# Optimization experiments

Measured on AMD Instinct MI355X. Metric: run time of the kernel, lower is better.

The kernel has to match this reference:

```python
import jax, jax.numpy as jnp
import numpy as np

BETA = 4.0  # temperature of soft cluster assignment in filling loss


def _pairwise_sq_dist(a, b):
    # a: [N,D], b: [K,D] -> [N,K] squared euclidean distances
    return (jnp.sum(a * a, -1, keepdims=True)
            - 2.0 * (a @ b.T)
            + jnp.sum(b * b, -1)[None, :])


def setup_inputs() -> dict:
    key = jax.random.key(0)
    k1, k2, k3, k4 = jax.random.split(key, 4)
    N, D, K = 131072, 64, 16
    x = jax.random.normal(k1, (N, D), jnp.float32)
    cluster_centers = jax.random.normal(k2, (K, D), jnp.float32)
    target = jax.random.normal(k3, (N, D), jnp.float32)
    ft = jax.random.uniform(k4, (K,), jnp.float32)
    filling_target = ft / ft.sum()
    # prediction = kmeans assignment of the fixed target set (computed once, constant)
    prediction = jnp.argmin(_pairwise_sq_dist(target, cluster_centers), axis=-1)
    return {"x": x, "cluster_centers": cluster_centers,
            "filling_target": filling_target, "target": target,
            "prediction": prediction}


def reference(x, cluster_centers, filling_target, target, prediction):
    N, D = x.shape
    Nt = target.shape[0]
    K = cluster_centers.shape[0]
    BIG = jnp.finfo(x.dtype).max  # padding value that sorts to the end

    d2 = _pairwise_sq_dist(x, cluster_centers)  # [N,K]

    # --- cluster filling MSE: soft assignment fractions vs filling_target ---
    soft = jax.nn.softmax(-BETA * d2, axis=-1)          # [N,K]
    filling = soft.mean(axis=0)                          # [K]
    loss_fil = jnp.mean((filling - filling_target) ** 2)

    # --- per-cluster sorted (per-dimension 1D) Wasserstein distance ---
    pred_x = jax.lax.stop_gradient(jnp.argmin(d2, axis=-1))  # kmeans_predict(x).detach()
    L = min(N, Nt)  # static upper bound on per-cluster min_size
    rows = jnp.arange(L)

    loss_med = jnp.zeros((), x.dtype)
    for k in range(K):  # fixed structural loop over clusters
        mx = pred_x == k
        mt = prediction == k
        m = jnp.minimum(mx.sum(), mt.sum())  # min_size (dynamic value, static shapes)
        # keep only the FIRST m members (original order), as x[in_cluster][:m]
        keep_x = mx & ((jnp.cumsum(mx) - 1) < m)
        keep_t = mt & ((jnp.cumsum(mt) - 1) < m)
        # mask out non-members with BIG so they sort to the bottom, sort per dim
        xs = jnp.sort(jnp.where(keep_x[:, None], x, BIG), axis=0)[:L]       # [L,D]
        ts = jnp.sort(jnp.where(keep_t[:, None], target, BIG), axis=0)[:L]  # [L,D]
        valid = (rows < m)[:, None]                                          # [L,1]
        diff = jnp.where(valid, jnp.abs(xs - ts), 0.0)
        # mean(|sort(x) - sort(y)|) over the m x D selected elements
        denom = (m * D).astype(x.dtype)
        loss_med = loss_med + jnp.where(m > 0, diff.sum() / denom, 0.0)

    return loss_fil + loss_med
```

## Files before the change

### kernel.cpp

```cpp
#include <hip/hip_runtime.h>
#include <stdint.h>

#define N_ROWS 131072
#define DIMS 64
#define KCL 16
#define BETA 4.0f
#define NBLK 512
#define CHUNK 16384
#define STH 1024
#define SEG_STRIDE 263168
#define VOFF (1u<<21)

typedef unsigned long long u64;
typedef unsigned int u32;

__device__ __forceinline__ u32 enc_f(float f) {
  u32 u = __float_as_uint(f);
  return (u & 0x80000000u) ? ~u : (u | 0x80000000u);
}
__device__ __forceinline__ float dec_f(u32 e) {
  u32 u = (e & 0x80000000u) ? (e & 0x7FFFFFFFu) : ~e;
  return __uint_as_float(u);
}
__device__ __forceinline__ u32 U4(u32 u) { return u ^ ((u >> 3) & 7u); }

#define CS(a,b,dd) { u32 _mn = min(a,b), _mx = max(a,b); a = (dd)?_mn:_mx; b = (dd)?_mx:_mn; }
#define CSV(A,B,D) { CS(A.x,B.x,D) CS(A.y,B.y,D) CS(A.z,B.z,D) CS(A.w,B.w,D) }

#define M16G(a,b,c,d,e,f,g,h,i2,j2,k2,l,m,n,o,p,D) \
  CS(a,i2,D) CS(b,j2,D) CS(c,k2,D) CS(d,l,D) CS(e,m,D) CS(f,n,D) CS(g,o,D) CS(h,p,D) \
  CS(a,e,D)  CS(b,f,D)  CS(c,g,D)  CS(d,h,D) CS(i2,m,D) CS(j2,n,D) CS(k2,o,D) CS(l,p,D) \
  CS(a,c,D)  CS(b,d,D)  CS(e,g,D)  CS(f,h,D) CS(i2,k2,D) CS(j2,l,D) CS(m,o,D) CS(n,p,D) \
  CS(a,b,D)  CS(c,d,D)  CS(e,f,D)  CS(g,h,D) CS(i2,j2,D) CS(k2,l,D) CS(m,n,D) CS(o,p,D)

#define SORT16G(a,b,c,d,e,f,g,h,i2,j2,k2,l,m,n,o,p,D) \
  CS(a,b,D) CS(c,d,!(D)) CS(e,f,D) CS(g,h,!(D)) CS(i2,j2,D) CS(k2,l,!(D)) CS(m,n,D) CS(o,p,!(D)) \
  CS(a,c,D) CS(b,d,D) CS(e,g,!(D)) CS(f,h,!(D)) CS(i2,k2,D) CS(j2,l,D) CS(m,o,!(D)) CS(n,p,!(D)) \
  CS(a,b,D) CS(c,d,D) CS(e,f,!(D)) CS(g,h,!(D)) CS(i2,j2,D) CS(k2,l,D) CS(m,n,!(D)) CS(o,p,!(D)) \
  CS(a,e,D) CS(b,f,D) CS(c,g,D) CS(d,h,D) CS(i2,m,!(D)) CS(j2,n,!(D)) CS(k2,o,!(D)) CS(l,p,!(D)) \
  CS(a,c,D) CS(b,d,D) CS(e,g,D) CS(f,h,D) CS(i2,k2,!(D)) CS(j2,l,!(D)) CS(m,o,!(D)) CS(n,p,!(D)) \
  CS(a,b,D) CS(c,d,D) CS(e,f,D) CS(g,h,D) CS(i2,j2,!(D)) CS(k2,l,!(D)) CS(m,n,!(D)) CS(o,p,!(D)) \
  M16G(a,b,c,d,e,f,g,h,i2,j2,k2,l,m,n,o,p,D)

#define MERGE16F(D) M16G(r0,r1,r2,r3,r4,r5,r6,r7,r8,r9,r10,r11,r12,r13,r14,r15,D)
#define SORT16F(D)  SORT16G(r0,r1,r2,r3,r4,r5,r6,r7,r8,r9,r10,r11,r12,r13,r14,r15,D)

#define LOADTILE16(src) \
  { uint4 _a0=src[U4(ub+0)],_a1=src[U4(ub+1)],_a2=src[U4(ub+2)],_a3=src[U4(ub+3)]; \
    r0=_a0.x;r1=_a0.y;r2=_a0.z;r3=_a0.w; r4=_a1.x;r5=_a1.y;r6=_a1.z;r7=_a1.w; \
    r8=_a2.x;r9=_a2.y;r10=_a2.z;r11=_a2.w; r12=_a3.x;r13=_a3.y;r14=_a3.z;r15=_a3.w; }

#define STORETILE16(dst) \
  { dst[U4(ub+0)]=make_uint4(r0,r1,r2,r3);   dst[U4(ub+1)]=make_uint4(r4,r5,r6,r7); \
    dst[U4(ub+2)]=make_uint4(r8,r9,r10,r11); dst[U4(ub+3)]=make_uint4(r12,r13,r14,r15); }

__device__ __forceinline__ void wave_tail(uint4* lds4, u32 RU, u32 Lw, u32 gbase,
                                          u32 k, u32 jtop, u32 lane)
{
  u32 j = jtop;
  while (j >= 32u) {
    u32 ud = j >> 3;
    if (lane < (Lw >> 4)) {
      u32 bu = RU + (((lane & ~(ud - 1u)) << 2) | (lane & (ud - 1u)));
      bool up = (((gbase + (bu << 2)) & k) == 0u);
      uint4 A0 = lds4[U4(bu)],           A1 = lds4[U4(bu + ud)],
            A2 = lds4[U4(bu + 2u * ud)], A3 = lds4[U4(bu + 3u * ud)];
      CSV(A0,A2,up) CSV(A1,A3,up)
      CSV(A0,A1,up) CSV(A2,A3,up)
      lds4[U4(bu)] = A0;           lds4[U4(bu + ud)] = A1;
      lds4[U4(bu + 2u * ud)] = A2; lds4[U4(bu + 3u * ud)] = A3;
    }
    j >>= 2;
  }
  if (j == 16u) {
    u32 total = Lw >> 3;
    for (u32 inst = lane; inst < total; inst += 64u) {
      u32 bu = RU + (((inst & ~3u) << 1) | (inst & 3u));
      bool up = (((gbase + (bu << 2)) & k) == 0u);
      uint4 A = lds4[U4(bu)], B = lds4[U4(bu + 4u)];
      CSV(A,B,up)
      lds4[U4(bu)] = A; lds4[U4(bu + 4u)] = B;
    }
  }
}

__device__ __forceinline__ void cross1(uint4* lds4, u32 Wn, u32 gb, u32 k, u32 jtop, u32 tid)
{
  u32 ud = jtop >> 2;
  u32 total = Wn >> 3;
  for (u32 inst = tid; inst < total; inst += STH) {
    u32 bu = ((inst & ~(ud - 1u)) << 1) | (inst & (ud - 1u));
    bool up = (((gb + (bu << 2)) & k) == 0u);
    uint4 A = lds4[U4(bu)], B = lds4[U4(bu + ud)];
    CSV(A,B,up)
    lds4[U4(bu)] = A; lds4[U4(bu + ud)] = B;
  }
}
__device__ __forceinline__ void cross2(uint4* lds4, u32 Wn, u32 gb, u32 k, u32 jtop, u32 tid)
{
  u32 ud = jtop >> 3;
  u32 total = Wn >> 4;
  for (u32 inst = tid; inst < total; inst += STH) {
    u32 bu = ((inst & ~(ud - 1u)) << 2) | (inst & (ud - 1u));
    bool up = (((gb + (bu << 2)) & k) == 0u);
    uint4 A0 = lds4[U4(bu)],            A1 = lds4[U4(bu + ud)],
          A2 = lds4[U4(bu + 2u * ud)],  A3 = lds4[U4(bu + 3u * ud)];
    CSV(A0,A2,up) CSV(A1,A3,up)
    CSV(A0,A1,up) CSV(A2,A3,up)
    lds4[U4(bu)] = A0;           lds4[U4(bu + ud)] = A1;
    lds4[U4(bu + 2u * ud)] = A2; lds4[U4(bu + 3u * ud)] = A3;
  }
}
__device__ __forceinline__ void cross3(uint4* lds4, u32 Wn, u32 gb, u32 k, u32 jtop, u32 tid)
{
  u32 ud = jtop >> 4;
  u32 total = Wn >> 5;
  for (u32 inst = tid; inst < total; inst += STH) {
    u32 bu = ((inst & ~(ud - 1u)) << 3) | (inst & (ud - 1u));
    bool up = (((gb + (bu << 2)) & k) == 0u);
    uint4 A0 = lds4[U4(bu)],            A1 = lds4[U4(bu + ud)],
          A2 = lds4[U4(bu + 2u * ud)],  A3 = lds4[U4(bu + 3u * ud)],
          A4 = lds4[U4(bu + 4u * ud)],  A5 = lds4[U4(bu + 5u * ud)],
          A6 = lds4[U4(bu + 6u * ud)],  A7 = lds4[U4(bu + 7u * ud)];
    CSV(A0,A4,up) CSV(A1,A5,up) CSV(A2,A6,up) CSV(A3,A7,up)
    CSV(A0,A2,up) CSV(A1,A3,up) CSV(A4,A6,up) CSV(A5,A7,up)
    CSV(A0,A1,up) CSV(A2,A3,up) CSV(A4,A5,up) CSV(A6,A7,up)
    lds4[U4(bu)] = A0;           lds4[U4(bu + ud)] = A1;
    lds4[U4(bu + 2u * ud)] = A2; lds4[U4(bu + 3u * ud)] = A3;
    lds4[U4(bu + 4u * ud)] = A4; lds4[U4(bu + 5u * ud)] = A5;
    lds4[U4(bu + 6u * ud)] = A6; lds4[U4(bu + 7u * ud)] = A7;
  }
}

__global__ __launch_bounds__(256) void k_assign(
    const float* __restrict__ x, const float* __restrict__ centers,
    const int* __restrict__ predT, int* __restrict__ predX,
    float* __restrict__ fill_sum, u32* __restrict__ histX, u32* __restrict__ histT)
{
  __shared__ float c[KCL][DIMS];
  __shared__ float cn[KCL];
  __shared__ float fs[KCL];
  __shared__ u32 hx[KCL], ht[KCL];
  int tid = threadIdx.x;
  for (int t = tid; t < KCL * DIMS; t += 256) c[t / DIMS][t % DIMS] = centers[t];
  if (tid < KCL) { fs[tid] = 0.f; hx[tid] = 0; ht[tid] = 0; }
  __syncthreads();
  if (tid < KCL) {
    float s = 0.f;
    for (int d = 0; d < DIMS; ++d) s += c[tid][d] * c[tid][d];
    cn[tid] = s;
  }
  __syncthreads();
  int i = blockIdx.x * 256 + tid;
  const float4* xr = (const float4*)(x + (size_t)i * DIMS);
  float dot[KCL];
#pragma unroll
  for (int k = 0; k < KCL; ++k) dot[k] = 0.f;
  for (int t = 0; t < DIMS / 4; ++t) {
    float4 v = xr[t];
#pragma unroll
    for (int k = 0; k < KCL; ++k)
      dot[k] += v.x * c[k][4 * t] + v.y * c[k][4 * t + 1] + v.z * c[k][4 * t + 2] + v.w * c[k][4 * t + 3];
  }
  float sc[KCL];
  float smin = 3.0e38f; int kmin = 0;
#pragma unroll
  for (int k = 0; k < KCL; ++k) {
    sc[k] = cn[k] - 2.f * dot[k];
    if (sc[k] < smin) { smin = sc[k]; kmin = k; }
  }
  float e[KCL]; float esum = 0.f;
#pragma unroll
  for (int k = 0; k < KCL; ++k) { e[k] = expf(-BETA * (sc[k] - smin)); esum += e[k]; }
  float inv = 1.f / esum;
#pragma unroll
  for (int k = 0; k < KCL; ++k) atomicAdd(&fs[k], e[k] * inv);
  predX[i] = kmin;
  atomicAdd(&hx[kmin], 1u);
  atomicAdd(&ht[predT[i]], 1u);
  __syncthreads();
  if (tid < KCL) {
    histX[blockIdx.x * KCL + tid] = hx[tid];
    histT[blockIdx.x * KCL + tid] = ht[tid];
    atomicAdd(&fill_sum[tid], fs[tid]);
  }
}

__global__ __launch_bounds__(512) void k_scan(
    const u32* __restrict__ histX, const u32* __restrict__ histT,
    u32* __restrict__ baseX, u32* __restrict__ baseT,
    const float* __restrict__ fill_sum, const float* __restrict__ ftarget,
    int* __restrict__ m_out, float* __restrict__ w_out,
    int* __restrict__ p_out, int* __restrict__ pOff_out, int* __restrict__ mOff_out,
    int* __restrict__ nlo_out, float* __restrict__ loss_fil)
{
  __shared__ u32 part[2][KCL][17];
  __shared__ u32 tot[2][KCL];
  __shared__ float sq[KCL];
  __shared__ int sp[KCL];
  __shared__ int smv[KCL];
  int tid = threadIdx.x;
  int side = tid >> 8;
  int rem = tid & 255;
  int c = rem >> 4;
  int sub = rem & 15;
  const u32* hist = side ? histT : histX;
  u32* base = side ? baseT : baseX;
  int b0 = sub * 32;
  u32 s = 0;
  for (int b = b0; b < b0 + 32; ++b) s += hist[b * KCL + c];
  part[side][c][sub] = s;
  __syncthreads();
  if (sub == 0) {
    u32 run = 0;
    for (int t = 0; t < 16; ++t) { u32 v = part[side][c][t]; part[side][c][t] = run; run += v; }
    tot[side][c] = run;
  }
  __syncthreads();
  u32 run = part[side][c][sub];
  for (int b = b0; b < b0 + 32; ++b) { base[b * KCL + c] = run; run += hist[b * KCL + c]; }
  if (tid < KCL) {
    int m = min((int)tot[0][tid], (int)tot[1][tid]);
    m_out[tid] = m;
    smv[tid] = m;
    w_out[tid] = (m > 0) ? 1.f / ((float)m * (float)DIMS) : 0.f;
    int pp = 32;
    while (pp < m) pp <<= 1;
    sp[tid] = pp;
    p_out[tid] = pp;
    int nlo = 0;
    if (pp > CHUNK) {
      int nch = pp / CHUNK;
      for (int j = 1; j < nch; j += 2) {
        int v = m - j * CHUNK;
        if (v < 0) v = 0;
        if (v > CHUNK) v = CHUNK;
        nlo += CHUNK - v;
      }
    }
    nlo_out[tid] = nlo;
    float d = fill_sum[tid] / (float)N_ROWS - ftarget[tid];
    sq[tid] = d * d;
  }
  __syncthreads();
  if (tid == 0) {
    float s2 = 0.f;
    int acc = 0, macc = 0;
    for (int k = 0; k < KCL; ++k) {
      s2 += sq[k];
      pOff_out[k] = acc;
      acc += sp[k];
      mOff_out[k] = macc;
      macc += smv[k];
    }
    pOff_out[KCL] = acc;
    mOff_out[KCL] = macc;
    *loss_fil = s2 / (float)KCL;
  }
}

__global__ __launch_bounds__(256) void k_rank(
    const int* __restrict__ predX, const int* __restrict__ predT,
    const u32* __restrict__ baseX, const u32* __restrict__ baseT,
    const int* __restrict__ mG, const int* __restrict__ mOffG,
    int* __restrict__ idxX, int* __restrict__ idxT)
{
  __shared__ int wcX[4][KCL], wcT[4][KCL];
  __shared__ int smo[KCL], sm2[KCL];
  int tid = threadIdx.x;
  int lane = tid & 63, wave = tid >> 6;
  if (tid < KCL) { smo[tid] = mOffG[tid]; sm2[tid] = mG[tid]; }
  int i = blockIdx.x * 256 + tid;
  int kx = predX[i], kt = predT[i];
  u64 below = (1ull << lane) - 1ull;
  int lrX = 0, lrT = 0;
  for (int cc = 0; cc < KCL; ++cc) {
    u64 mx = __ballot(kx == cc);
    u64 mt = __ballot(kt == cc);
    if (kx == cc) lrX = __popcll(mx & below);
    if (kt == cc) lrT = __popcll(mt & below);
    if (lane == 0) { wcX[wave][cc] = __popcll(mx); wcT[wave][cc] = __popcll(mt); }
  }
  __syncthreads();
  int wbX = 0, wbT = 0;
  for (int w2 = 0; w2 < wave; ++w2) { wbX += wcX[w2][kx]; wbT += wcT[w2][kt]; }
  int rX = (int)baseX[blockIdx.x * KCL + kx] + wbX + lrX;
  int rT = (int)baseT[blockIdx.x * KCL + kt] + wbT + lrT;
  if (rX < sm2[kx]) idxX[smo[kx] + rX] = i;
  if (rT < sm2[kt]) idxT[smo[kt] + rT] = i;
}

__global__ __launch_bounds__(256) void k_gather(
    const float* __restrict__ x, const float* __restrict__ tgt,
    const int* __restrict__ idxX, const int* __restrict__ idxT,
    const int* __restrict__ pOffG, const int* __restrict__ mOffG,
    const int* __restrict__ mG, const int* __restrict__ pG,
    u32* __restrict__ valX, u32* __restrict__ valT, int d0, int Dbc)
{
  __shared__ int spOff[KCL + 1];
  __shared__ int smo[KCL], sm2[KCL], sp2[KCL];
  int tid = threadIdx.x;
  if (tid <= KCL) spOff[tid] = pOffG[tid];
  if (tid < KCL) { smo[tid] = mOffG[tid]; sm2[tid] = mG[tid]; sp2[tid] = pG[tid]; }
  __syncthreads();
  int pos = blockIdx.x * 256 + tid;
  if (pos >= spOff[KCL]) return;
  int c = 0;
#pragma unroll
  for (int cc = 1; cc < KCL; ++cc) c += (pos >= spOff[cc]) ? 1 : 0;
  int rel = pos - spOff[c];
  u32* dx = valX + pos;
  u32* dt = valT + pos;
  if (rel < sm2[c]) {
    int w = smo[c] + rel;
    int iX = idxX[w], iT = idxT[w];
    if ((Dbc & 3) == 0) {
      const float4* xr = (const float4*)(x + (size_t)iX * DIMS + d0);
      const float4* tr = (const float4*)(tgt + (size_t)iT * DIMS + d0);
      for (int q = 0; q < (Dbc >> 2); ++q) {
        float4 a = xr[q];
        float4 b = tr[q];
        size_t base = (size_t)(4 * q) * SEG_STRIDE;
        dx[base]                  = enc_f(a.x);
        dx[base + SEG_STRIDE]     = enc_f(a.y);
        dx[base + 2 * (size_t)SEG_STRIDE] = enc_f(a.z);
        dx[base + 3 * (size_t)SEG_STRIDE] = enc_f(a.w);
        dt[base]                  = enc_f(b.x);
        dt[base + SEG_STRIDE]     = enc_f(b.y);
        dt[base + 2 * (size_t)SEG_STRIDE] = enc_f(b.z);
        dt[base + 3 * (size_t)SEG_STRIDE] = enc_f(b.w);
      }
    } else {
      const float* xr = x + (size_t)iX * DIMS + d0;
      const float* tr = tgt + (size_t)iT * DIMS + d0;
      for (int d = 0; d < Dbc; ++d) {
        dx[(size_t)d * SEG_STRIDE] = enc_f(xr[d]);
        dt[(size_t)d * SEG_STRIDE] = enc_f(tr[d]);
      }
    }
  } else {
    u32 pv = (sp2[c] > CHUNK && ((rel >> 14) & 1)) ? 0u : 0xFFFFFFFFu;
    for (int d = 0; d < Dbc; ++d) {
      dx[(size_t)d * SEG_STRIDE] = pv;
      dt[(size_t)d * SEG_STRIDE] = pv;
    }
  }
}

__global__ __launch_bounds__(STH, 8) void k_sort(
    u32* __restrict__ vbase, const int* __restrict__ pG, const int* __restrict__ pOffG,
    const int* __restrict__ mG)
{
  __shared__ __align__(16) u32 lds[CHUNK];
  uint4* lds4 = (uint4*)lds;
  int t = blockIdx.x, c = -1, sub = 0, acc = 0;
  for (int cc = 0; cc < KCL; ++cc) {
    int pc0 = pG[cc];
    int nc = (pc0 > CHUNK) ? (pc0 / CHUNK) : 1;
    if (t < acc + nc) { c = cc; sub = t - acc; break; }
    acc += nc;
  }
  if (c < 0) return;
  int pc = pG[c];
  u32 CH = (u32)min(pc, CHUNK);
  u32 gb = (u32)sub * (u32)CHUNK;
  int v = mG[c] - (int)gb;
  if (v > (int)CH) v = (int)CH;
  if (v <= 0) return;
  u32 W = 32u;
  while (W < (u32)v) W <<= 1;
  if (W > CH) W = CH;
  bool desc = (pc > CHUNK) && (sub & 1);
  u32 inv = desc ? 0xFFFFFFFFu : 0u;
  u32* seg = vbase + (size_t)blockIdx.y * SEG_STRIDE + pOffG[c] + gb;
  uint4* gp4 = (uint4*)seg;
  u32 tid = threadIdx.x;
  u32 lane = tid & 63u;
  u32 wv = tid >> 6;
  u32 ub = tid << 2;
  u32 bas = tid << 4;
  bool act = (bas < W);
  u32 RU = wv << 8;
  u32 runBase = wv << 10;
  bool wact = (runBase < W);
  u32 Lw = W - runBase; if (Lw > 1024u) Lw = 1024u;
  u32 r0,r1,r2,r3,r4,r5,r6,r7,r8,r9,r10,r11,r12,r13,r14,r15;

  if (act) {
    uint4 a0 = gp4[ub + 0], a1 = gp4[ub + 1], a2 = gp4[ub + 2], a3 = gp4[ub + 3];
    r0 = a0.x^inv; r1 = a0.y^inv; r2  = a0.z^inv; r3  = a0.w^inv;
    r4 = a1.x^inv; r5 = a1.y^inv; r6  = a1.z^inv; r7  = a1.w^inv;
    r8 = a2.x^inv; r9 = a2.y^inv; r10 = a2.z^inv; r11 = a2.w^inv;
    r12 = a3.x^inv; r13 = a3.y^inv; r14 = a3.z^inv; r15 = a3.w^inv;
    bool D = ((bas & 16u) == 0u);
    SORT16F(D);
    STORETILE16(lds4);
  }
  if (wact) {
    for (u32 k = 32u; k <= Lw; k <<= 1) {
      wave_tail(lds4, RU, Lw, 0u, k, k >> 1, lane);
      if (act) {
        LOADTILE16(lds4);
        bool D = ((bas & k) == 0u);
        MERGE16F(D);
        STORETILE16(lds4);
      }
    }
  }

  if (W >= 2048u) {
    __syncthreads();
    for (u32 k = 2048u; k <= W; k <<= 1) {
      u32 jt = k >> 1;
      if (jt >= 8192u) {
        cross3(lds4, W, 0u, k, 8192u, tid);
        __syncthreads();
        cross1(lds4, W, 0u, k, 1024u, tid);
        __syncthreads();
      } else if (jt == 4096u) {
        cross3(lds4, W, 0u, k, 4096u, tid);
        __syncthreads();
      } else if (jt == 2048u) {
        cross2(lds4, W, 0u, k, 2048u, tid);
        __syncthreads();
      } else {
        cross1(lds4, W, 0u, k, 1024u, tid);
        __syncthreads();
      }
      if (wact) {
        wave_tail(lds4, RU, Lw, 0u, k, 512u, lane);
        if (act) {
          LOADTILE16(lds4);
          bool D = ((bas & k) == 0u);
          MERGE16F(D);
          STORETILE16(lds4);
        }
      }
      if (k < W) __syncthreads();
    }
  }

  __syncthreads();
  for (u32 uu = tid; (uu << 2) < W; uu += STH) {
    uint4 q = lds4[U4(uu)];
    q.x ^= inv; q.y ^= inv; q.z ^= inv; q.w ^= inv;
    gp4[uu] = q;
  }
}

__global__ __launch_bounds__(256) void k_gpass(
    u32* __restrict__ vbase, const int* __restrict__ pG, const int* __restrict__ pOffG,
    int kk, int j)
{
  u32* base = vbase + (size_t)blockIdx.y * SEG_STRIDE;
  int pb[KCL]; int tot = 0;
#pragma unroll
  for (int c = 0; c < KCL; ++c) {
    pb[c] = tot;
    int pc = pG[c];
    if (pc >= kk) tot += pc >> 1;
  }
  for (int g4 = (blockIdx.x * 256 + threadIdx.x) << 2; g4 < tot; g4 += gridDim.x * 256 * 4) {
    int c = 0;
#pragma unroll
    for (int cc = 1; cc < KCL; ++cc) c += (g4 >= pb[cc]) ? 1 : 0;
    int u = g4 - pb[c];
    int i = ((u & ~(j - 1)) << 1) | (u & (j - 1));
    bool up = ((i & kk) == 0);
    u32* s2 = base + pOffG[c];
    uint4 A = *(const uint4*)(s2 + i);
    uint4 B = *(const uint4*)(s2 + i + j);
    CS(A.x, B.x, up) CS(A.y, B.y, up) CS(A.z, B.z, up) CS(A.w, B.w, up)
    *(uint4*)(s2 + i) = A;
    *(uint4*)(s2 + i + j) = B;
  }
}

__global__ __launch_bounds__(STH) void k_gfinish(
    u32* __restrict__ vbase, const int* __restrict__ pG, const int* __restrict__ pOffG, int kk)
{
  __shared__ __align__(16) u32 lds[CHUNK];
  uint4* lds4 = (uint4*)lds;
  int t = blockIdx.x, c = -1, sub = 0, acc = 0;
  for (int cc = 0; cc < KCL; ++cc) {
    int pc = pG[cc];
    if (pc < kk) continue;
    int nc = pc / CHUNK;
    if (t < acc + nc) { c = cc; sub = t - acc; break; }
    acc += nc;
  }
  if (c < 0) return;
  u32 gb = (u32)sub * (u32)CHUNK;
  u32* seg = vbase + (size_t)blockIdx.y * SEG_STRIDE + pOffG[c] + gb;
  uint4* gp4 = (uint4*)seg;
  u32 tid = threadIdx.x;
  u32 lane = tid & 63u;
  u32 wv = tid >> 6;
  u32 RU = wv << 8;
  u32 ub = tid << 2;
  u32 bas = tid << 4;
  u32 r0,r1,r2,r3,r4,r5,r6,r7,r8,r9,r10,r11,r12,r13,r14,r15;

  for (u32 uu = tid; uu < CHUNK / 4; uu += STH) lds4[U4(uu)] = gp4[uu];
  __syncthreads();
  cross3(lds4, (u32)CHUNK, gb, (u32)kk, 8192u, tid);
  __syncthreads();
  cross1(lds4, (u32)CHUNK, gb, (u32)kk, 1024u, tid);
  __syncthreads();
  wave_tail(lds4, RU, 1024u, gb, (u32)kk, 512u, lane);
  {
    LOADTILE16(lds4);
    bool up = (((gb + bas) & (u32)kk) == 0u);
    MERGE16F(up);
    STORETILE16(lds4);
  }
  __syncthreads();
  for (u32 uu = tid; uu < CHUNK / 4; uu += STH) gp4[uu] = lds4[U4(uu)];
}

__global__ __launch_bounds__(256) void k_reduce(
    const u32* __restrict__ valX, const u32* __restrict__ valT,
    const int* __restrict__ pOffG, const int* __restrict__ mOffG,
    const int* __restrict__ nloG,
    const float* __restrict__ wG, float* __restrict__ lossAcc)
{
  __shared__ int spOff[KCL];
  __shared__ int smo[KCL + 1];
  __shared__ int snlo[KCL];
  __shared__ float swt[KCL];
  __shared__ float red[256];
  int tid = threadIdx.x;
  if (tid <= KCL) smo[tid] = mOffG[tid];
  if (tid < KCL) { spOff[tid] = pOffG[tid]; snlo[tid] = nloG[tid]; swt[tid] = wG[tid]; }
  __syncthreads();
  int d = blockIdx.y;
  const u32* vx = valX + (size_t)d * SEG_STRIDE;
  const u32* vt = valT + (size_t)d * SEG_STRIDE;
  int M = smo[KCL];
  float s = 0.f;
  for (int w = blockIdx.x * 256 + tid; w < M; w += gridDim.x * 256) {
    int c = 0;
#pragma unroll
    for (int cc = 1; cc < KCL; ++cc) c += (w >= smo[cc]) ? 1 : 0;
    int pos = spOff[c] + snlo[c] + (w - smo[c]);
    float a = dec_f(vx[pos]), b = dec_f(vt[pos]);
    s += fabsf(a - b) * swt[c];
  }
  red[tid] = s;
  __syncthreads();
  for (int st = 128; st > 0; st >>= 1) {
    if (tid < st) red[tid] += red[tid + st];
    __syncthreads();
  }
  if (tid == 0) atomicAdd(lossAcc, red[0]);
}

__global__ void k_final(const float* __restrict__ lossAcc, const float* __restrict__ loss_fil,
                        float* __restrict__ out)
{
  out[0] = *lossAcc + *loss_fil;
}

extern "C" void kernel_launch(void* const* d_in, const int* in_sizes, int n_in,
                              void* d_out, int out_size, void* d_ws, size_t ws_size,
                              hipStream_t stream)
{
  const float* x       = (const float*)d_in[0];
  const float* centers = (const float*)d_in[1];
  const float* ftarget = (const float*)d_in[2];
  const float* tgt     = (const float*)d_in[3];
  const int*   predT   = (const int*)d_in[4];
  float* out = (float*)d_out;

  char* ws = (char*)d_ws;
  float* fill_sum = (float*)(ws + 0);
  float* lossAcc  = (float*)(ws + 64);
  float* loss_fil = (float*)(ws + 68);
  int*   m_buf    = (int*)(ws + 128);
  float* w_buf    = (float*)(ws + 192);
  int*   p_buf    = (int*)(ws + 256);
  int*   pOff     = (int*)(ws + 320);
  int*   mOff     = (int*)(ws + 400);
  u32* histX = (u32*)(ws + 512);
  u32* histT = (u32*)(ws + 512 + 32768);
  u32* baseX = (u32*)(ws + 512 + 65536);
  u32* baseT = (u32*)(ws + 512 + 98304);
  int* predX = (int*)(ws + 131584);
  int* idxX  = (int*)(ws + 655872);
  int* idxT  = (int*)(ws + 1180160);
  int* nlo_buf = (int*)(ws + 1704448);
  u32* vbase = (u32*)(ws + VOFF);

  size_t avail_elems = (ws_size > VOFF) ? ((ws_size - VOFF) / 4) : 0;
  int Db = (int)(avail_elems / (2ull * SEG_STRIDE));
  if (Db > DIMS) Db = DIMS;
  if (Db >= 4) Db &= ~3;
  if (Db < 1) Db = 1;

  hipMemsetAsync(ws, 0, 128, stream);
  k_assign<<<NBLK, 256, 0, stream>>>(x, centers, predT, predX, fill_sum, histX, histT);
  k_scan<<<1, 512, 0, stream>>>(histX, histT, baseX, baseT, fill_sum, ftarget,
                                m_buf, w_buf, p_buf, pOff, mOff, nlo_buf, loss_fil);
  k_rank<<<NBLK, 256, 0, stream>>>(predX, predT, baseX, baseT, m_buf, mOff, idxX, idxT);

  for (int d0 = 0; d0 < DIMS; d0 += Db) {
    int Dbc = (Db < DIMS - d0) ? Db : (DIMS - d0);
    u32* valX = vbase;
    u32* valT = vbase + (size_t)Dbc * SEG_STRIDE;
    k_gather<<<1028, 256, 0, stream>>>(x, tgt, idxX, idxT, pOff, mOff, m_buf, p_buf,
                                       valX, valT, d0, Dbc);
    k_sort<<<dim3(34, 2 * Dbc), STH, 0, stream>>>(vbase, p_buf, pOff, m_buf);
    for (int kk = 2 * CHUNK; kk <= N_ROWS; kk <<= 1) {
      int gx = (kk == 2 * CHUNK) ? 32 : 8;
      for (int j = kk >> 1; j >= CHUNK; j >>= 1)
        k_gpass<<<dim3(gx, 2 * Dbc), 256, 0, stream>>>(vbase, p_buf, pOff, kk, j);
      k_gfinish<<<dim3(32, 2 * Dbc), STH, 0, stream>>>(vbase, p_buf, pOff, kk);
    }
    k_reduce<<<dim3(32, Dbc), 256, 0, stream>>>(valX, valT, pOff, mOff, nlo_buf,
                                                w_buf, lossAcc);
  }
  k_final<<<1, 1, 0, stream>>>(lossAcc, loss_fil, out);
}
```

Baseline: 728.7 us.

## Stage gather through LDS transpose and trim sort/finish grid sizes

```diff
diff --git a/kernel.cpp b/kernel.cpp
--- a/kernel.cpp
+++ b/kernel.cpp
@@ -299,44 +299,75 @@
 {
   __shared__ int spOff[KCL + 1];
   __shared__ int smo[KCL], sm2[KCL], sp2[KCL];
+  __shared__ float pl[32][257];
+  __shared__ int sRowX[256], sRowT[256];
+  __shared__ u32 sPv[256];
   int tid = threadIdx.x;
   if (tid <= KCL) spOff[tid] = pOffG[tid];
   if (tid < KCL) { smo[tid] = mOffG[tid]; sm2[tid] = mG[tid]; sp2[tid] = pG[tid]; }
   __syncthreads();
   int pos = blockIdx.x * 256 + tid;
-  if (pos >= spOff[KCL]) return;
-  int c = 0;
-#pragma unroll
-  for (int cc = 1; cc < KCL; ++cc) c += (pos >= spOff[cc]) ? 1 : 0;
-  int rel = pos - spOff[c];
+  bool inr = pos < spOff[KCL];
+  int c = 0, rel = 0;
+  bool vld = false;
+  if (inr) {
+#pragma unroll
+    for (int cc = 1; cc < KCL; ++cc) c += (pos >= spOff[cc]) ? 1 : 0;
+    rel = pos - spOff[c];
+    vld = rel < sm2[c];
+  }
+
+  if (Dbc == 64) {
+    int w = vld ? (smo[c] + rel) : 0;
+    sRowX[tid] = vld ? idxX[w] : -1;
+    sRowT[tid] = vld ? idxT[w] : -1;
+    sPv[tid] = inr ? ((sp2[c] > CHUNK && ((rel >> 14) & 1)) ? 0u : 0xFFFFFFFFu) : 0u;
+    __syncthreads();
+#pragma unroll
+    for (int side = 0; side < 2; ++side) {
+      const float* src = side ? tgt : x;
+      const int* sRow = side ? sRowT : sRowX;
+      u32* dst = side ? valT : valX;
+#pragma unroll
+      for (int h = 0; h < 2; ++h) {
+        int h0 = h * 32;
+        for (int idx = tid; idx < 256 * 8; idx += 256) {
+          int r = idx >> 3, f = idx & 7;
+          int row = sRow[r];
+          if (row >= 0) {
+            float4 v = *(const float4*)(src + (size_t)row * DIMS + d0 + h0 + f * 4);
+            pl[f * 4 + 0][r] = v.x;
+            pl[f * 4 + 1][r] = v.y;
+            pl[f * 4 + 2][r] = v.z;
+            pl[f * 4 + 3][r] = v.w;
+          }
+        }
+        __syncthreads();
+        if (inr) {
+          bool v2 = sRow[tid] >= 0;
+          u32 pv = sPv[tid];
+          for (int dl = 0; dl < 32; ++dl) {
+            u32 e = v2 ? enc_f(pl[dl][tid]) : pv;
+            dst[(size_t)(h0 + dl) * SEG_STRIDE + pos] = e;
+          }
+        }
+        __syncthreads();
+      }
+    }
+    return;
+  }
+
+  if (!inr) return;
   u32* dx = valX + pos;
   u32* dt = valT + pos;
-  if (rel < sm2[c]) {
+  if (vld) {
     int w = smo[c] + rel;
     int iX = idxX[w], iT = idxT[w];
-    if ((Dbc & 3) == 0) {
-      const float4* xr = (const float4*)(x + (size_t)iX * DIMS + d0);
-      const float4* tr = (const float4*)(tgt + (size_t)iT * DIMS + d0);
-      for (int q = 0; q < (Dbc >> 2); ++q) {
-        float4 a = xr[q];
-        float4 b = tr[q];
-        size_t base = (size_t)(4 * q) * SEG_STRIDE;
-        dx[base]                  = enc_f(a.x);
-        dx[base + SEG_STRIDE]     = enc_f(a.y);
-        dx[base + 2 * (size_t)SEG_STRIDE] = enc_f(a.z);
-        dx[base + 3 * (size_t)SEG_STRIDE] = enc_f(a.w);
-        dt[base]                  = enc_f(b.x);
-        dt[base + SEG_STRIDE]     = enc_f(b.y);
-        dt[base + 2 * (size_t)SEG_STRIDE] = enc_f(b.z);
-        dt[base + 3 * (size_t)SEG_STRIDE] = enc_f(b.w);
-      }
-    } else {
-      const float* xr = x + (size_t)iX * DIMS + d0;
-      const float* tr = tgt + (size_t)iT * DIMS + d0;
-      for (int d = 0; d < Dbc; ++d) {
-        dx[(size_t)d * SEG_STRIDE] = enc_f(xr[d]);
-        dt[(size_t)d * SEG_STRIDE] = enc_f(tr[d]);
-      }
+    const float* xr = x + (size_t)iX * DIMS + d0;
+    const float* tr = tgt + (size_t)iT * DIMS + d0;
+    for (int d = 0; d < Dbc; ++d) {
+      dx[(size_t)d * SEG_STRIDE] = enc_f(xr[d]);
+      dt[(size_t)d * SEG_STRIDE] = enc_f(tr[d]);
     }
   } else {
     u32 pv = (sp2[c] > CHUNK && ((rel >> 14) & 1)) ? 0u : 0xFFFFFFFFu;
@@ -609,12 +640,12 @@
     u32* valT = vbase + (size_t)Dbc * SEG_STRIDE;
     k_gather<<<1028, 256, 0, stream>>>(x, tgt, idxX, idxT, pOff, mOff, m_buf, p_buf,
                                        valX, valT, d0, Dbc);
-    k_sort<<<dim3(34, 2 * Dbc), STH, 0, stream>>>(vbase, p_buf, pOff, m_buf);
+    k_sort<<<dim3(28, 2 * Dbc), STH, 0, stream>>>(vbase, p_buf, pOff, m_buf);
     for (int kk = 2 * CHUNK; kk <= N_ROWS; kk <<= 1) {
       int gx = (kk == 2 * CHUNK) ? 32 : 8;
       for (int j = kk >> 1; j >= CHUNK; j >>= 1)
         k_gpass<<<dim3(gx, 2 * Dbc), 256, 0, stream>>>(vbase, p_buf, pOff, kk, j);
-      k_gfinish<<<dim3(32, 2 * Dbc), STH, 0, stream>>>(vbase, p_buf, pOff, kk);
+      k_gfinish<<<dim3(18, 2 * Dbc), STH, 0, stream>>>(vbase, p_buf, pOff, kk);
     }
     k_reduce<<<dim3(32, Dbc), 256, 0, stream>>>(valX, valT, pOff, mOff, nlo_buf,
                                                 w_buf, lossAcc);
```

New measurement: 599.3 us. 1.22x faster.
